# Kernel optimization log

Measured on AMD Instinct MI355X. Metric: run time of the kernel, lower is better.

Reference implementation:

```python
import jax, jax.numpy as jnp
import numpy as np

D_MODEL = 512
DFF = 2048
TOP_K = 2
EXPERTS_PER_LEVEL = (4, 8)  # hierarchical MoE: 2 levels


def setup_inputs() -> dict:
    key = jax.random.key(0)
    ks = jax.random.split(key, 12)
    def w(k, fan_in, shape):
        return jax.random.normal(k, shape, jnp.float32) * (1.0 / np.sqrt(fan_in))
    def b(k, shape):
        return jax.random.normal(k, shape, jnp.float32) * 0.01
    E0, E1 = EXPERTS_PER_LEVEL
    return {
        "x": jax.random.normal(ks[0], (4, 2048, D_MODEL), jnp.float32),
        # level 0: router + 4 experts (stacked along leading expert axis)
        "Wr0": w(ks[1], D_MODEL, (D_MODEL, E0)),
        "W1_0": w(ks[2], D_MODEL, (E0, D_MODEL, DFF)),
        "b1_0": b(ks[3], (E0, DFF)),
        "W2_0": w(ks[4], DFF, (E0, DFF, D_MODEL)),
        "b2_0": b(ks[5], (E0, D_MODEL)),
        # level 1: router + 8 experts
        "Wr1": w(ks[6], D_MODEL, (D_MODEL, E1)),
        "W1_1": w(ks[7], D_MODEL, (E1, D_MODEL, DFF)),
        "b1_1": b(ks[8], (E1, DFF)),
        "W2_1": w(ks[9], DFF, (E1, DFF, D_MODEL)),
        "b2_1": b(ks[10], (E1, D_MODEL)),
    }


def _moe_level(x, Wr, W1, b1, W2, b2, k):
    # Router: full softmax probs over experts; dispatch = binary top-k mask.
    probs = jax.nn.softmax(jnp.einsum('bsd,de->bse', x, Wr), axis=-1)  # [B,S,E]
    _, top_idx = jax.lax.top_k(probs, k)                               # [B,S,k]
    dispatch = jax.nn.one_hot(top_idx, probs.shape[-1], dtype=x.dtype).sum(axis=-2)  # [B,S,E]
    # Faithful to the source: every expert FFN runs on the MASKED inputs
    # (x * dispatch), then is combined with the FULL router probs.
    xm = x[:, :, None, :] * dispatch[..., None]                        # [B,S,E,D]
    h = jax.nn.relu(jnp.einsum('bsed,edf->bsef', xm, W1) + b1)         # [B,S,E,DFF]
    y = jnp.einsum('bsef,efd->bsed', h, W2) + b2                       # [B,S,E,D]
    return jnp.sum(y * probs[..., None], axis=2)                       # [B,S,D]


def reference(x, Wr0, W1_0, b1_0, W2_0, b2_0, Wr1, W1_1, b1_1, W2_1, b2_1):
    # inference path: dropout is identity, no capacity adaptation
    h0 = _moe_level(x, Wr0, W1_0, b1_0, W2_0, b2_0, TOP_K)
    out = _moe_level(h0, Wr1, W1_1, b1_1, W2_1, b2_1, TOP_K)
    return out
```

## Files before the change

kernel.cpp:

```cpp
#include <hip/hip_runtime.h>
#include <hip/hip_bf16.h>
#include <math.h>

#define TOK   8192
#define DM    512
#define DFFN  2048
#define NE0   4
#define NE1   8

typedef __bf16 bf16;
typedef __bf16 bf16x8 __attribute__((ext_vector_type(8)));
typedef float  f32x4  __attribute__((ext_vector_type(4)));

__device__ __forceinline__ double wave_sum_f64(double v){
#pragma unroll
  for (int o = 32; o > 0; o >>= 1) v += __shfl_down(v, o, 64);
  return v;
}
__device__ __forceinline__ float wave_sum_f32(float v){
#pragma unroll
  for (int o = 32; o > 0; o >>= 1) v += __shfl_down(v, o, 64);
  return v;
}

__device__ __forceinline__ void gload16(const bf16* g, bf16* l){
  __builtin_amdgcn_global_load_lds(
      (const __attribute__((address_space(1))) void*)g,
      (__attribute__((address_space(3))) void*)l, 16, 0, 0);
}

__global__ void f32_to_bf16(const float* __restrict__ in, bf16* __restrict__ out, int n){
  int i = blockIdx.x*256 + threadIdx.x;
  if (i < n) out[i] = (bf16)in[i];
}

__global__ void transpose_convert(const float* __restrict__ in, bf16* __restrict__ hi,
                                  bf16* __restrict__ lo, int K, int N){
  __shared__ float tile[64][65];
  int e  = blockIdx.z;
  int n0 = blockIdx.x*64, k0 = blockIdx.y*64;
  const float* src = in + (size_t)e*K*N;
  int c = threadIdx.x & 63, r4 = threadIdx.x >> 6;
#pragma unroll
  for (int i = 0; i < 16; ++i){
    int r = r4*16 + i;
    tile[r][c] = src[(size_t)(k0 + r)*N + n0 + c];
  }
  __syncthreads();
  bf16* dh = hi + (size_t)e*K*N;
  bf16* dl = lo ? (lo + (size_t)e*K*N) : nullptr;
#pragma unroll
  for (int i = 0; i < 16; ++i){
    int r = r4*16 + i;
    float v = tile[c][r];
    size_t o = (size_t)(n0 + r)*K + k0 + c;
    bf16 h = (bf16)v;
    dh[o] = h;
    if (dl) dl[o] = (bf16)(v - (float)h);
  }
}

__global__ void compute_c(const float* __restrict__ W2, const float* __restrict__ b1,
                          const float* __restrict__ b2, float* __restrict__ c){
  int gid = blockIdx.x*256 + threadIdx.x;
  int e = gid >> 9, d = gid & (DM-1);
  int fc = blockIdx.y;
  float acc = (fc == 0) ? b2[gid] : 0.f;
  const float* w  = W2 + (size_t)e*DFFN*DM + (size_t)fc*256*DM + d;
  const float* bb = b1 + e*DFFN + fc*256;
#pragma unroll 4
  for (int f = 0; f < 256; ++f) acc += fmaxf(bb[f], 0.f) * w[(size_t)f*DM];
  atomicAdd(&c[gid], acc);
}

__global__ void compute_M(const float* __restrict__ W2_0, const float* __restrict__ Wr1,
                          float* __restrict__ M, int nrows){
  int wv = threadIdx.x >> 6, lane = threadIdx.x & 63;
  int row = blockIdx.x*4 + wv;
  if (row >= nrows) return;
  const float* w = W2_0 + (size_t)row*DM + lane*8;
  float w8[8];
#pragma unroll
  for (int q = 0; q < 8; ++q) w8[q] = w[q];
  double acc[8] = {0,0,0,0,0,0,0,0};
#pragma unroll
  for (int q = 0; q < 8; ++q){
    const float* wr = Wr1 + (size_t)(lane*8 + q)*NE1;
#pragma unroll
    for (int p = 0; p < 8; ++p) acc[p] += (double)w8[q]*(double)wr[p];
  }
#pragma unroll
  for (int p = 0; p < 8; ++p) acc[p] = wave_sum_f64(acc[p]);
  if (lane == 0){
#pragma unroll
    for (int p = 0; p < 8; ++p) M[(size_t)row*8 + p] = (float)acc[p];
  }
}

__global__ void compute_cb_proj(const float* __restrict__ c0, const float* __restrict__ b2_0,
                                const float* __restrict__ Wr1, double* __restrict__ c0p,
                                double* __restrict__ b2p){
  int t = threadIdx.x;
  if (t >= NE0*NE1) return;
  int e = t >> 3, p = t & 7;
  double a = 0.0, b = 0.0;
  for (int d = 0; d < DM; ++d){
    double w = (double)Wr1[d*NE1 + p];
    a += (double)c0[e*DM + d]  * w;
    b += (double)b2_0[e*DM + d]* w;
  }
  c0p[t] = a; b2p[t] = b;
}

__global__ void prefix_offs(const int* __restrict__ counts, int NE, int* __restrict__ offs){
  if (threadIdx.x == 0){
    int s = 0;
    for (int e = 0; e < NE; ++e){ offs[e] = s; s += counts[e]; }
    offs[NE] = s;
  }
}

__global__ void router0_kernel(const float* __restrict__ x, const float* __restrict__ Wr0,
                               float* __restrict__ probs0, int* __restrict__ idx0,
                               bf16* __restrict__ xhi, bf16* __restrict__ xlo){
  int wv = threadIdx.x >> 6, lane = threadIdx.x & 63;
  int t = blockIdx.x*4 + wv;
  const float* xr = x + (size_t)t*DM + lane*8;
  float xv[8];
#pragma unroll
  for (int i = 0; i < 8; ++i) xv[i] = xr[i];
  bf16x8 hv, lv;
#pragma unroll
  for (int i = 0; i < 8; ++i){
    bf16 h = (bf16)xv[i];
    hv[i] = h;
    lv[i] = (bf16)(xv[i] - (float)h);
  }
  *(bf16x8*)(xhi + (size_t)t*DM + lane*8) = hv;
  *(bf16x8*)(xlo + (size_t)t*DM + lane*8) = lv;

  double lg[NE0];
#pragma unroll
  for (int e = 0; e < NE0; ++e){
    double s = 0.0;
#pragma unroll
    for (int i = 0; i < 8; ++i) s += (double)xv[i] * (double)Wr0[(lane*8 + i)*NE0 + e];
    lg[e] = wave_sum_f64(s);
  }
  if (lane == 0){
    double m = lg[0];
#pragma unroll
    for (int e = 1; e < NE0; ++e) m = fmax(m, lg[e]);
    double den = 0.0, ex[NE0];
#pragma unroll
    for (int e = 0; e < NE0; ++e){ ex[e] = exp(lg[e] - m); den += ex[e]; }
    float pf[NE0];
#pragma unroll
    for (int e = 0; e < NE0; ++e){ pf[e] = (float)(ex[e]/den); probs0[t*NE0 + e] = pf[e]; }
    int e0 = 0;
#pragma unroll
    for (int e = 1; e < NE0; ++e) if (pf[e] > pf[e0]) e0 = e;
    int e1 = (e0 == 0) ? 1 : 0;
#pragma unroll
    for (int e = 0; e < NE0; ++e) if (e != e0 && pf[e] > pf[e1]) e1 = e;
    idx0[t*2 + 0] = e0; idx0[t*2 + 1] = e1;
  }
}

__global__ void router1_kernel(const float* __restrict__ proj, const float* __restrict__ probs0,
                               const int* __restrict__ idx0, const double* __restrict__ c0p,
                               const double* __restrict__ b2p, float* __restrict__ probs1,
                               int* __restrict__ idx1){
  int t = blockIdx.x*256 + threadIdx.x;
  float p0[NE0];
#pragma unroll
  for (int e = 0; e < NE0; ++e) p0[e] = probs0[t*NE0 + e];
  double lg[NE1];
#pragma unroll
  for (int p = 0; p < NE1; ++p){
    double s = 0.0;
#pragma unroll
    for (int e = 0; e < NE0; ++e) s += (double)p0[e] * c0p[e*NE1 + p];
    lg[p] = s;
  }
#pragma unroll
  for (int sl = 0; sl < 2; ++sl){
    int e = idx0[t*2 + sl];
    double pe = (double)p0[e];
    const float* pr = proj + ((size_t)(sl*TOK + t))*NE1;
#pragma unroll
    for (int p = 0; p < NE1; ++p) lg[p] += pe * ((double)pr[p] + b2p[e*NE1 + p] - c0p[e*NE1 + p]);
  }
  double m = lg[0];
#pragma unroll
  for (int p = 1; p < NE1; ++p) m = fmax(m, lg[p]);
  double den = 0.0, ex[NE1];
#pragma unroll
  for (int p = 0; p < NE1; ++p){ ex[p] = exp(lg[p] - m); den += ex[p]; }
  float pf[NE1];
#pragma unroll
  for (int p = 0; p < NE1; ++p){ pf[p] = (float)(ex[p]/den); probs1[t*NE1 + p] = pf[p]; }
  int e0 = 0;
#pragma unroll
  for (int p = 1; p < NE1; ++p) if (pf[p] > pf[e0]) e0 = p;
  int e1 = (e0 == 0) ? 1 : 0;
#pragma unroll
  for (int p = 0; p < NE1; ++p) if (p != e0 && pf[p] > pf[e1]) e1 = p;
  idx1[t*2 + 0] = e0; idx1[t*2 + 1] = e1;
}

__global__ void build_lists(const int* __restrict__ idx, int NE,
                            int* __restrict__ list, int* __restrict__ counts){
  __shared__ int lcnt[8];
  __shared__ int lbase[8];
  const int tid = threadIdx.x, lane = tid & 63;
  if (tid < NE) lcnt[tid] = 0;
  __syncthreads();
  const int g = blockIdx.x*1024 + tid;
  const int slot = g >> 13;
  const int t = g & (TOK-1);
  const int e = idx[t*2 + slot];
  int wbase = 0, rank = 0;
  for (int ee = 0; ee < NE; ++ee){
    unsigned long long m = __ballot(e == ee);
    if (e == ee){
      int leader = __builtin_ctzll(m);
      int b = 0;
      if (lane == leader) b = atomicAdd(&lcnt[ee], (int)__popcll(m));
      wbase = __shfl(b, leader, 64);
      rank  = (int)__popcll(m & ((1ull << lane) - 1ull));
    }
  }
  __syncthreads();
  if (tid < NE) lbase[tid] = atomicAdd(&counts[tid], lcnt[tid]);
  __syncthreads();
  list[e*TOK + lbase[e] + wbase + rank] = slot*TOK + t;
}

__global__ void init_combine(const float* __restrict__ probs, const float* __restrict__ c,
                             int NE, float* __restrict__ tgt){
  int gid = blockIdx.x*256 + threadIdx.x;
  int t = gid >> 9, d = gid & (DM-1);
  float v = 0.f;
  for (int e = 0; e < NE; ++e) v += probs[t*NE + e] * c[e*DM + d];
  tgt[gid] = v;
}

__global__ void proj_from_h(const bf16* __restrict__ Hb, const bf16* __restrict__ Hlo,
                            int FC, int f0, const float* __restrict__ Mproj,
                            const int* __restrict__ list, const int* __restrict__ offs,
                            float* __restrict__ proj){
  int wv = threadIdx.x >> 6, lane = threadIdx.x & 63;
  int rr = blockIdx.x*4 + wv;
  if (rr >= offs[NE0]) return;
  int e = 0;
#pragma unroll
  for (int k = 1; k < NE0; ++k) if (rr >= offs[k]) e = k;
  int r = list[e*TOK + (rr - offs[e])];
  const bf16* hh = Hb  + (size_t)rr*FC;
  const bf16* hl = Hlo + (size_t)rr*FC;
  const float* Me = Mproj + ((size_t)e*DFFN + f0)*8;
  float acc[8] = {0,0,0,0,0,0,0,0};
  for (int c = 0; c < FC; c += 512){
    int fl = c + lane*8;
    if (fl < FC){
      bf16x8 a = *(const bf16x8*)(hh + fl);
      bf16x8 b = *(const bf16x8*)(hl + fl);
#pragma unroll
      for (int q = 0; q < 8; ++q){
        float hv = (float)a[q] + (float)b[q];
        const f32x4* mp = (const f32x4*)(Me + (size_t)(fl + q)*8);
        f32x4 m0 = mp[0], m1 = mp[1];
#pragma unroll
        for (int p = 0; p < 4; ++p){
          acc[p]   += hv * m0[p];
          acc[4+p] += hv * m1[p];
        }
      }
    }
  }
#pragma unroll
  for (int p = 0; p < 8; ++p) acc[p] = wave_sum_f32(acc[p]);
  if (lane == 0){
#pragma unroll
    for (int p = 0; p < 8; ++p) proj[(size_t)r*8 + p] += acc[p];
  }
}


template<int SPLIT>
__global__ __launch_bounds__(256, 2) void gemm_ffn1(
    const bf16* __restrict__ Ahi, const bf16* __restrict__ Alo,
    const bf16* __restrict__ Bhi, const bf16* __restrict__ Blo,
    const float* __restrict__ b1,
    const int* __restrict__ list, const int* __restrict__ counts,
    const int* __restrict__ offs,
    bf16* __restrict__ Hb, bf16* __restrict__ Hlo, int f0, int FC)
{
  constexpr int BUFE  = SPLIT ? 16384 : 8192;
  constexpr int SMEME = (2*BUFE > 17408) ? 2*BUFE : 17408;
  __shared__ alignas(16) bf16 smem[SMEME];

  const int e   = blockIdx.z;
  const int cnt = counts[e];
  const int bx = blockIdx.x, by = blockIdx.y;
  int xl, yl;
  if (gridDim.y == 16){
    xl = ((by >> 1) << 3) + (bx >> 3);
    yl = ((bx & 7) << 1) + (by & 1);
  } else { xl = bx; yl = by; }
  const int m0 = xl * 128;
  if (m0 >= cnt) return;
  const int rbase = offs[e] + m0;
  const int n0  = yl * 128;
  const int ng0 = f0 + n0;

  const int tid  = threadIdx.x;
  const int lane = tid & 63, wv = tid >> 6;
  const int wm = wv >> 1, wn = wv & 1;
  const int quad = lane >> 4, l15 = lane & 15;
  const int* le = list + e*TOK;

  const int strow = tid >> 2;
  const int ch8   = (((tid & 3) ^ ((tid >> 3) & 3)) << 3);
  int growR[2];
#pragma unroll
  for (int p = 0; p < 2; ++p){
    int m = m0 + p*64 + strow;
    growR[p] = (m < cnt) ? (le[m] & (TOK-1)) : 0;
  }
  const bf16* Bh = Bhi + (size_t)e*DFFN*DM;
  const bf16* Bl = SPLIT ? (Blo + (size_t)e*DFFN*DM) : nullptr;

  f32x4 acc[4][4];
#pragma unroll
  for (int i = 0; i < 4; ++i)
#pragma unroll
    for (int j = 0; j < 4; ++j) acc[i][j] = (f32x4){0.f,0.f,0.f,0.f};

  const int swzl = (l15 >> 1) & 3;
  int aPos[4], bPos[4];
#pragma unroll
  for (int i = 0; i < 4; ++i){
    aPos[i] = (wm*256 + (i*16 + l15)*4 + (quad ^ swzl)) * 8;
    bPos[i] = (wn*256 + (i*16 + l15)*4 + (quad ^ swzl)) * 8;
  }

  auto stage = [&](int ks, int buf){
    const int colo = (ks << 5) + ch8;
    bf16* dst = smem + buf*BUFE;
#pragma unroll
    for (int p = 0; p < 2; ++p){
      gload16(Ahi + (size_t)growR[p]*DM + colo,                  dst +         (p*256 + tid)*8);
      gload16(Bh  + (size_t)(ng0 + p*64 + strow)*DM + colo,      dst + 4096  + (p*256 + tid)*8);
      if (SPLIT){
        gload16(Alo + (size_t)growR[p]*DM + colo,                dst + 8192  + (p*256 + tid)*8);
        gload16(Bl  + (size_t)(ng0 + p*64 + strow)*DM + colo,    dst + 12288 + (p*256 + tid)*8);
      }
    }
  };

  constexpr int NIT = DM/32;
  stage(0, 0);
  stage(1, 1);
  int cur = 0;
  for (int ks = 0; ks < NIT; ++ks){
    if (ks + 1 < NIT){
      if (SPLIT) asm volatile("s_waitcnt vmcnt(8)" ::: "memory");
      else       asm volatile("s_waitcnt vmcnt(4)" ::: "memory");
    } else {
      asm volatile("s_waitcnt vmcnt(0)" ::: "memory");
    }
    __builtin_amdgcn_sched_barrier(0);
    __builtin_amdgcn_s_barrier();
    __builtin_amdgcn_sched_barrier(0);
    const bf16* B0 = smem + cur*BUFE;
    bf16x8 ah[4], bh[4];
#pragma unroll
    for (int i = 0; i < 4; ++i){
      ah[i] = *(const bf16x8*)&B0[aPos[i]];
      bh[i] = *(const bf16x8*)&B0[4096 + bPos[i]];
    }
#pragma unroll
    for (int i = 0; i < 4; ++i)
#pragma unroll
      for (int j = 0; j < 4; ++j)
        acc[i][j] = __builtin_amdgcn_mfma_f32_16x16x32_bf16(ah[i], bh[j], acc[i][j], 0,0,0);
    if (SPLIT){
      bf16x8 t2[4];
#pragma unroll
      for (int i = 0; i < 4; ++i) t2[i] = *(const bf16x8*)&B0[12288 + bPos[i]];
#pragma unroll
      for (int i = 0; i < 4; ++i)
#pragma unroll
        for (int j = 0; j < 4; ++j)
          acc[i][j] = __builtin_amdgcn_mfma_f32_16x16x32_bf16(ah[i], t2[j], acc[i][j], 0,0,0);
#pragma unroll
      for (int i = 0; i < 4; ++i) t2[i] = *(const bf16x8*)&B0[8192 + aPos[i]];
#pragma unroll
      for (int i = 0; i < 4; ++i)
#pragma unroll
        for (int j = 0; j < 4; ++j)
          acc[i][j] = __builtin_amdgcn_mfma_f32_16x16x32_bf16(t2[i], bh[j], acc[i][j], 0,0,0);
    }
    asm volatile("s_waitcnt lgkmcnt(0)" ::: "memory");
    __builtin_amdgcn_sched_barrier(0);
    __builtin_amdgcn_s_barrier();
    __builtin_amdgcn_sched_barrier(0);
    if (ks + 2 < NIT) stage(ks + 2, cur);
    cur ^= 1;
  }

  float bjv[4];
#pragma unroll
  for (int j = 0; j < 4; ++j)
    bjv[j] = b1[e*DFFN + ng0 + wn*64 + j*16 + l15];

  bf16* Cs = smem;
#pragma unroll
  for (int i = 0; i < 4; ++i)
#pragma unroll
    for (int j = 0; j < 4; ++j)
#pragma unroll
      for (int reg = 0; reg < 4; ++reg){
        float h = fmaxf(acc[i][j][reg] + bjv[j], 0.f);
        Cs[(wm*64 + i*16 + quad*4 + reg)*136 + wn*64 + j*16 + l15] = (bf16)h;
      }
  __syncthreads();
  {
    const int srow = tid >> 1, shalf = (tid & 1) * 64;
    if (m0 + srow < cnt){
      bf16* dst = Hb + (size_t)(rbase + srow)*FC + n0 + shalf;
      const bf16* srcl = &Cs[srow*136 + shalf];
#pragma unroll
      for (int q = 0; q < 8; ++q)
        *(bf16x8*)(dst + q*8) = *(const bf16x8*)(srcl + q*8);
    }
  }
  if (SPLIT){
    __syncthreads();
#pragma unroll
    for (int i = 0; i < 4; ++i)
#pragma unroll
      for (int j = 0; j < 4; ++j)
#pragma unroll
        for (int reg = 0; reg < 4; ++reg){
          float h = fmaxf(acc[i][j][reg] + bjv[j], 0.f);
          bf16 hi = (bf16)h;
          Cs[(wm*64 + i*16 + quad*4 + reg)*136 + wn*64 + j*16 + l15] = (bf16)(h - (float)hi);
        }
    __syncthreads();
    const int srow = tid >> 1, shalf = (tid & 1) * 64;
    if (m0 + srow < cnt){
      bf16* dst = Hlo + (size_t)(rbase + srow)*FC + n0 + shalf;
      const bf16* srcl = &Cs[srow*136 + shalf];
#pragma unroll
      for (int q = 0; q < 8; ++q)
        *(bf16x8*)(dst + q*8) = *(const bf16x8*)(srcl + q*8);
    }
  }
}

__global__ __launch_bounds__(256, 3) void gemm_ffn2(
    const bf16* __restrict__ Hb, int FC, int f0,
    const bf16* __restrict__ Bt,
    const float* __restrict__ b2, const float* __restrict__ ce,
    const float* __restrict__ probs, int NE,
    const int* __restrict__ list, const int* __restrict__ counts,
    const int* __restrict__ offs,
    float* __restrict__ tgt, int addBias)
{
  __shared__ alignas(16) bf16 smem[16384];

  const int e   = blockIdx.z;
  const int cnt = counts[e];
  const int bx = blockIdx.x, by = blockIdx.y;
  const int xl = (bx >> 3) + (((bx & 1) + (by << 1)) << 3);
  const int yl = (bx & 7) >> 1;
  const int m0 = xl*128;
  if (m0 >= cnt) return;
  const int rbase = offs[e];
  const int n0  = yl*128;

  const int tid = threadIdx.x, lane = tid & 63, wv = tid >> 6;
  const int wm = wv >> 1, wn = wv & 1, quad = lane >> 4, l15 = lane & 15;
  const int* le = list + e*TOK;

  const int strow = tid >> 2;
  const int ch8   = (((tid & 3) ^ ((tid >> 3) & 3)) << 3);
  int growR[2];
#pragma unroll
  for (int p = 0; p < 2; ++p){
    int m = m0 + p*64 + strow;
    growR[p] = rbase + ((m < cnt) ? m : (cnt - 1));
  }
  const bf16* Be = Bt + (size_t)e*DM*DFFN;

  f32x4 acc[4][4];
#pragma unroll
  for (int i = 0; i < 4; ++i)
#pragma unroll
    for (int j = 0; j < 4; ++j) acc[i][j] = (f32x4){0.f,0.f,0.f,0.f};

  const int swzl = (l15 >> 1) & 3;
  int aPos[4], bPos[4];
#pragma unroll
  for (int i = 0; i < 4; ++i){
    aPos[i] = (wm*256 + (i*16 + l15)*4 + (quad ^ swzl)) * 8;
    bPos[i] = (wn*256 + (i*16 + l15)*4 + (quad ^ swzl)) * 8;
  }

  auto stage = [&](int ks, int buf){
    const int colo = (ks << 5) + ch8;
    bf16* dst = smem + buf*8192;
#pragma unroll
    for (int p = 0; p < 2; ++p){
      gload16(Hb + (size_t)growR[p]*FC + colo,                       dst +        (p*256 + tid)*8);
      gload16(Be + (size_t)(n0 + p*64 + strow)*DFFN + f0 + colo,     dst + 4096 + (p*256 + tid)*8);
    }
  };

  const int NIT = FC/32;
  stage(0, 0);
  stage(1, 1);
  int cur = 0;
  for (int ks = 0; ks < NIT; ++ks){
    if (ks + 1 < NIT) asm volatile("s_waitcnt vmcnt(4)" ::: "memory");
    else              asm volatile("s_waitcnt vmcnt(0)" ::: "memory");
    __builtin_amdgcn_sched_barrier(0);
    __builtin_amdgcn_s_barrier();
    __builtin_amdgcn_sched_barrier(0);
    const bf16* B0 = smem + cur*8192;
    bf16x8 a[4], b[4];
#pragma unroll
    for (int i = 0; i < 4; ++i){
      a[i] = *(const bf16x8*)&B0[aPos[i]];
      b[i] = *(const bf16x8*)&B0[4096 + bPos[i]];
    }
#pragma unroll
    for (int i = 0; i < 4; ++i)
#pragma unroll
      for (int j = 0; j < 4; ++j)
        acc[i][j] = __builtin_amdgcn_mfma_f32_16x16x32_bf16(a[i], b[j], acc[i][j], 0,0,0);
    asm volatile("s_waitcnt lgkmcnt(0)" ::: "memory");
    __builtin_amdgcn_sched_barrier(0);
    __builtin_amdgcn_s_barrier();
    __builtin_amdgcn_sched_barrier(0);
    if (ks + 2 < NIT) stage(ks + 2, cur);
    cur ^= 1;
  }
#pragma unroll
  for (int i = 0; i < 4; ++i){
#pragma unroll
    for (int reg = 0; reg < 4; ++reg){
      int m = m0 + wm*64 + i*16 + quad*4 + reg;
      if (m >= cnt) continue;
      int r = le[m];
      int t = r & (TOK-1);
      float g = probs[t*NE + e];
#pragma unroll
      for (int j = 0; j < 4; ++j){
        int n = n0 + wn*64 + j*16 + l15;
        float v = acc[i][j][reg];
        if (addBias) v += b2[e*DM + n] - ce[e*DM + n];
        atomicAdd(&tgt[(size_t)t*DM + n], g*v);
      }
    }
  }
}

extern "C" void kernel_launch(void* const* d_in, const int* in_sizes, int n_in,
                              void* d_out, int out_size, void* d_ws, size_t ws_size,
                              hipStream_t stream)
{
  (void)in_sizes; (void)n_in; (void)out_size;
  const float* x    = (const float*)d_in[0];
  const float* Wr0  = (const float*)d_in[1];
  const float* W1_0 = (const float*)d_in[2];
  const float* b1_0 = (const float*)d_in[3];
  const float* W2_0 = (const float*)d_in[4];
  const float* b2_0 = (const float*)d_in[5];
  const float* Wr1  = (const float*)d_in[6];
  const float* W1_1 = (const float*)d_in[7];
  const float* b1_1 = (const float*)d_in[8];
  const float* W2_1 = (const float*)d_in[9];
  const float* b2_1 = (const float*)d_in[10];
  float* out = (float*)d_out;

  const size_t MB = (size_t)1 << 20;
  char* base = (char*)d_ws;

  bf16* xhi  = (bf16*)base;
  bf16* h0b  = (bf16*)base;
  bf16* xlo  = (bf16*)(base + 8*MB);
  bf16* w10h = (bf16*)(base + 16*MB);
  bf16* w10l = (bf16*)(base + 32*MB);
  bf16* w11h = (bf16*)(base + 16*MB);
  bf16* w21h = (bf16*)(base + 32*MB);
  bf16* w20h = (bf16*)(base + 48*MB);
  float* h0f = (float*)(base + 64*MB);

  char* mp = base + 80*MB;
  auto take = [&](size_t n) -> char* { char* p = mp; mp += (n + 255) & ~(size_t)255; return p; };
  float* probs0 = (float*)take((size_t)TOK*NE0*4);
  float* probs1 = (float*)take((size_t)TOK*NE1*4);
  int*   idx0   = (int*)  take((size_t)TOK*2*4);
  int*   idx1   = (int*)  take((size_t)TOK*2*4);
  int*   list0  = (int*)  take((size_t)NE0*TOK*4);
  int*   list1  = (int*)  take((size_t)NE1*TOK*4);
  int*   counts = (int*)  take(256);
  int*   offs0  = (int*)  take(256);
  int*   offs1  = (int*)  take(256);
  float* c0     = (float*)take((size_t)NE0*DM*4);
  float* c1     = (float*)take((size_t)NE1*DM*4);
  float* Mproj  = (float*)take((size_t)NE0*DFFN*NE1*4);
  double* c0p   = (double*)take(NE0*NE1*8);
  double* b2p   = (double*)take(NE0*NE1*8);
  float* proj   = (float*)take((size_t)2*TOK*NE1*4);

  const size_t fixed = 84*MB;
  int NCH;
  if      (ws_size >= fixed + 128*MB) NCH = 1;
  else if (ws_size >= fixed +  64*MB) NCH = 2;
  else if (ws_size >= fixed +  32*MB) NCH = 4;
  else if (ws_size >= fixed +  16*MB) NCH = 8;
  else return;
  const int FC = DFFN / NCH;
  const size_t chunkB = (size_t)2*TOK*FC*2;
  bf16* Hb   = (bf16*)(base + fixed);
  bf16* Hlo  = (bf16*)(base + fixed + chunkB);

  hipMemsetAsync(counts, 0, 16*sizeof(int), stream);
  hipMemsetAsync(c0, 0, (size_t)(NE0+NE1)*DM*4, stream);
  hipMemsetAsync(proj, 0, (size_t)2*TOK*NE1*4, stream);

  transpose_convert<<<dim3(DFFN/64, DM/64, NE0), 256, 0, stream>>>(W1_0, w10h, w10l, DM, DFFN);
  transpose_convert<<<dim3(DM/64, DFFN/64, NE0), 256, 0, stream>>>(W2_0, w20h, nullptr, DFFN, DM);
  compute_c<<<dim3(NE0*DM/256, 8), 256, 0, stream>>>(W2_0, b1_0, b2_0, c0);
  compute_c<<<dim3(NE1*DM/256, 8), 256, 0, stream>>>(W2_1, b1_1, b2_1, c1);
  compute_M<<<dim3(NE0*DFFN/4), 256, 0, stream>>>(W2_0, Wr1, Mproj, NE0*DFFN);
  compute_cb_proj<<<1, 64, 0, stream>>>(c0, b2_0, Wr1, c0p, b2p);

  router0_kernel<<<dim3(TOK/4), 256, 0, stream>>>(x, Wr0, probs0, idx0, xhi, xlo);
  build_lists<<<dim3(2*TOK/1024), 1024, 0, stream>>>(idx0, NE0, list0, counts);
  prefix_offs<<<1, 64, 0, stream>>>(counts, NE0, offs0);
  init_combine<<<dim3(TOK*DM/256), 256, 0, stream>>>(probs0, c0, NE0, h0f);
  for (int c = 0; c < NCH; ++c){
    gemm_ffn1<1><<<dim3(64, FC/128, NE0), 256, 0, stream>>>(
        xhi, xlo, w10h, w10l, b1_0, list0, counts, offs0, Hb, Hlo, c*FC, FC);
    proj_from_h<<<dim3(2*TOK/4), 256, 0, stream>>>(Hb, Hlo, FC, c*FC, Mproj,
                                                   list0, offs0, proj);
    gemm_ffn2<<<dim3(64, DM/128, NE0), 256, 0, stream>>>(
        Hb, FC, c*FC, w20h, b2_0, c0, probs0, NE0, list0, counts, offs0, h0f, (c == 0));
  }

  transpose_convert<<<dim3(DFFN/64, DM/64, NE1), 256, 0, stream>>>(W1_1, w11h, nullptr, DM, DFFN);
  transpose_convert<<<dim3(DM/64, DFFN/64, NE1), 256, 0, stream>>>(W2_1, w21h, nullptr, DFFN, DM);
  f32_to_bf16<<<dim3(TOK*DM/256), 256, 0, stream>>>(h0f, h0b, TOK*DM);
  router1_kernel<<<dim3(TOK/256), 256, 0, stream>>>(proj, probs0, idx0, c0p, b2p,
                                                    probs1, idx1);
  build_lists<<<dim3(2*TOK/1024), 1024, 0, stream>>>(idx1, NE1, list1, counts + NE0);
  prefix_offs<<<1, 64, 0, stream>>>(counts + NE0, NE1, offs1);
  init_combine<<<dim3(TOK*DM/256), 256, 0, stream>>>(probs1, c1, NE1, out);

  for (int c = 0; c < NCH; ++c){
    gemm_ffn1<0><<<dim3(64, FC/128, NE1), 256, 0, stream>>>(
        h0b, nullptr, w11h, nullptr, b1_1, list1, counts + NE0, offs1,
        Hb, nullptr, c*FC, FC);
    gemm_ffn2<<<dim3(64, DM/128, NE1), 256, 0, stream>>>(
        Hb, FC, c*FC, w21h, b2_1, c1, probs1, NE1, list1, counts + NE0, offs1, out, (c == 0));
  }
}
```

Measured before the change: 862.6 us.

## Replace atomic scatter-add in FFN2 epilogue with dense Y store plus gather combine

```diff
diff --git a/kernel.cpp b/kernel.cpp
--- a/kernel.cpp
+++ b/kernel.cpp
@@ -9,6 +9,7 @@
 #define NE1   8
 
 typedef __bf16 bf16;
+typedef __bf16 bf16x4 __attribute__((ext_vector_type(4)));
 typedef __bf16 bf16x8 __attribute__((ext_vector_type(8)));
 typedef float  f32x4  __attribute__((ext_vector_type(4)));
 
@@ -210,7 +211,8 @@
 }
 
 __global__ void build_lists(const int* __restrict__ idx, int NE,
-                            int* __restrict__ list, int* __restrict__ counts){
+                            int* __restrict__ list, int* __restrict__ counts,
+                            int* __restrict__ posn){
   __shared__ int lcnt[8];
   __shared__ int lbase[8];
   const int tid = threadIdx.x, lane = tid & 63;
@@ -234,7 +236,9 @@
   __syncthreads();
   if (tid < NE) lbase[tid] = atomicAdd(&counts[tid], lcnt[tid]);
   __syncthreads();
-  list[e*TOK + lbase[e] + wbase + rank] = slot*TOK + t;
+  const int p = lbase[e] + wbase + rank;
+  list[e*TOK + p] = slot*TOK + t;
+  posn[slot*TOK + t] = e*16384 + p;
 }
 
 __global__ void init_combine(const float* __restrict__ probs, const float* __restrict__ c,
@@ -244,6 +248,35 @@
   float v = 0.f;
   for (int e = 0; e < NE; ++e) v += probs[t*NE + e] * c[e*DM + d];
   tgt[gid] = v;
+}
+
+__global__ void gather_combine(const float* __restrict__ init, const float* __restrict__ Y,
+                               const int* __restrict__ posn, const int* __restrict__ offs,
+                               const float* __restrict__ probs, const float* __restrict__ b2,
+                               const float* __restrict__ ce, int NE,
+                               float* __restrict__ outF, bf16* __restrict__ outB){
+  int gid = blockIdx.x*256 + threadIdx.x;
+  int t = gid >> 7, d4 = (gid & 127) << 2;
+  f32x4 v = *(const f32x4*)(init + (size_t)t*DM + d4);
+#pragma unroll
+  for (int sl = 0; sl < 2; ++sl){
+    int pv = posn[sl*TOK + t];
+    int e = pv >> 14, p = pv & 16383;
+    int r = offs[e] + p;
+    float g = probs[t*NE + e];
+    f32x4 y  = *(const f32x4*)(Y  + (size_t)r*DM + d4);
+    f32x4 bb = *(const f32x4*)(b2 + (size_t)e*DM + d4);
+    f32x4 cc = *(const f32x4*)(ce + (size_t)e*DM + d4);
+#pragma unroll
+    for (int q = 0; q < 4; ++q) v[q] += g*(y[q] + bb[q] - cc[q]);
+  }
+  if (outF) *(f32x4*)(outF + (size_t)t*DM + d4) = v;
+  if (outB){
+    bf16x4 hb;
+#pragma unroll
+    for (int q = 0; q < 4; ++q) hb[q] = (bf16)v[q];
+    *(bf16x4*)(outB + (size_t)t*DM + d4) = hb;
+  }
 }
 
 __global__ void proj_from_h(const bf16* __restrict__ Hb, const bf16* __restrict__ Hlo,
@@ -468,7 +501,7 @@
     const float* __restrict__ probs, int NE,
     const int* __restrict__ list, const int* __restrict__ counts,
     const int* __restrict__ offs,
-    float* __restrict__ tgt, int addBias)
+    float* __restrict__ tgt, int addBias, float* __restrict__ Y)
 {
   __shared__ alignas(16) bf16 smem[16384];
 
@@ -549,21 +582,36 @@
     if (ks + 2 < NIT) stage(ks + 2, cur);
     cur ^= 1;
   }
-#pragma unroll
-  for (int i = 0; i < 4; ++i){
-#pragma unroll
-    for (int reg = 0; reg < 4; ++reg){
-      int m = m0 + wm*64 + i*16 + quad*4 + reg;
-      if (m >= cnt) continue;
-      int r = le[m];
-      int t = r & (TOK-1);
-      float g = probs[t*NE + e];
-#pragma unroll
-      for (int j = 0; j < 4; ++j){
-        int n = n0 + wn*64 + j*16 + l15;
-        float v = acc[i][j][reg];
-        if (addBias) v += b2[e*DM + n] - ce[e*DM + n];
-        atomicAdd(&tgt[(size_t)t*DM + n], g*v);
+  if (Y){
+#pragma unroll
+    for (int i = 0; i < 4; ++i){
+#pragma unroll
+      for (int reg = 0; reg < 4; ++reg){
+        int m = m0 + wm*64 + i*16 + quad*4 + reg;
+        if (m >= cnt) continue;
+        float* yr = Y + (size_t)(rbase + m)*DM + n0;
+#pragma unroll
+        for (int j = 0; j < 4; ++j)
+          yr[wn*64 + j*16 + l15] = acc[i][j][reg];
+      }
+    }
+  } else {
+#pragma unroll
+    for (int i = 0; i < 4; ++i){
+#pragma unroll
+      for (int reg = 0; reg < 4; ++reg){
+        int m = m0 + wm*64 + i*16 + quad*4 + reg;
+        if (m >= cnt) continue;
+        int r = le[m];
+        int t = r & (TOK-1);
+        float g = probs[t*NE + e];
+#pragma unroll
+        for (int j = 0; j < 4; ++j){
+          int n = n0 + wn*64 + j*16 + l15;
+          float v = acc[i][j][reg];
+          if (addBias) v += b2[e*DM + n] - ce[e*DM + n];
+          atomicAdd(&tgt[(size_t)t*DM + n], g*v);
+        }
       }
     }
   }
@@ -606,6 +654,8 @@
   float* probs1 = (float*)take((size_t)TOK*NE1*4);
   int*   idx0   = (int*)  take((size_t)TOK*2*4);
   int*   idx1   = (int*)  take((size_t)TOK*2*4);
+  int*   posn0  = (int*)  take((size_t)TOK*2*4);
+  int*   posn1  = (int*)  take((size_t)TOK*2*4);
   int*   list0  = (int*)  take((size_t)NE0*TOK*4);
   int*   list1  = (int*)  take((size_t)NE1*TOK*4);
   int*   counts = (int*)  take(256);
@@ -629,6 +679,8 @@
   const size_t chunkB = (size_t)2*TOK*FC*2;
   bf16* Hb   = (bf16*)(base + fixed);
   bf16* Hlo  = (bf16*)(base + fixed + chunkB);
+  const bool useY = (NCH == 1);
+  float* Ybuf = (float*)Hlo;
 
   hipMemsetAsync(counts, 0, 16*sizeof(int), stream);
   hipMemsetAsync(c0, 0, (size_t)(NE0+NE1)*DM*4, stream);
@@ -642,7 +694,7 @@
   compute_cb_proj<<<1, 64, 0, stream>>>(c0, b2_0, Wr1, c0p, b2p);
 
   router0_kernel<<<dim3(TOK/4), 256, 0, stream>>>(x, Wr0, probs0, idx0, xhi, xlo);
-  build_lists<<<dim3(2*TOK/1024), 1024, 0, stream>>>(idx0, NE0, list0, counts);
+  build_lists<<<dim3(2*TOK/1024), 1024, 0, stream>>>(idx0, NE0, list0, counts, posn0);
   prefix_offs<<<1, 64, 0, stream>>>(counts, NE0, offs0);
   init_combine<<<dim3(TOK*DM/256), 256, 0, stream>>>(probs0, c0, NE0, h0f);
   for (int c = 0; c < NCH; ++c){
@@ -651,15 +703,21 @@
     proj_from_h<<<dim3(2*TOK/4), 256, 0, stream>>>(Hb, Hlo, FC, c*FC, Mproj,
                                                    list0, offs0, proj);
     gemm_ffn2<<<dim3(64, DM/128, NE0), 256, 0, stream>>>(
-        Hb, FC, c*FC, w20h, b2_0, c0, probs0, NE0, list0, counts, offs0, h0f, (c == 0));
+        Hb, FC, c*FC, w20h, b2_0, c0, probs0, NE0, list0, counts, offs0, h0f, (c == 0),
+        useY ? Ybuf : nullptr);
   }
 
   transpose_convert<<<dim3(DFFN/64, DM/64, NE1), 256, 0, stream>>>(W1_1, w11h, nullptr, DM, DFFN);
   transpose_convert<<<dim3(DM/64, DFFN/64, NE1), 256, 0, stream>>>(W2_1, w21h, nullptr, DFFN, DM);
-  f32_to_bf16<<<dim3(TOK*DM/256), 256, 0, stream>>>(h0f, h0b, TOK*DM);
+  if (useY){
+    gather_combine<<<dim3(TOK*DM/4/256), 256, 0, stream>>>(
+        h0f, Ybuf, posn0, offs0, probs0, b2_0, c0, NE0, nullptr, h0b);
+  } else {
+    f32_to_bf16<<<dim3(TOK*DM/256), 256, 0, stream>>>(h0f, h0b, TOK*DM);
+  }
   router1_kernel<<<dim3(TOK/256), 256, 0, stream>>>(proj, probs0, idx0, c0p, b2p,
                                                     probs1, idx1);
-  build_lists<<<dim3(2*TOK/1024), 1024, 0, stream>>>(idx1, NE1, list1, counts + NE0);
+  build_lists<<<dim3(2*TOK/1024), 1024, 0, stream>>>(idx1, NE1, list1, counts + NE0, posn1);
   prefix_offs<<<1, 64, 0, stream>>>(counts + NE0, NE1, offs1);
   init_combine<<<dim3(TOK*DM/256), 256, 0, stream>>>(probs1, c1, NE1, out);
 
@@ -668,6 +726,11 @@
         h0b, nullptr, w11h, nullptr, b1_1, list1, counts + NE0, offs1,
         Hb, nullptr, c*FC, FC);
     gemm_ffn2<<<dim3(64, DM/128, NE1), 256, 0, stream>>>(
-        Hb, FC, c*FC, w21h, b2_1, c1, probs1, NE1, list1, counts + NE0, offs1, out, (c == 0));
-  }
-}
+        Hb, FC, c*FC, w21h, b2_1, c1, probs1, NE1, list1, counts + NE0, offs1, out, (c == 0),
+        useY ? Ybuf : nullptr);
+  }
+  if (useY){
+    gather_combine<<<dim3(TOK*DM/4/256), 256, 0, stream>>>(
+        out, Ybuf, posn1, offs1, probs1, b2_1, c1, NE1, out, nullptr);
+  }
+}
```

Measured after the change: 807.9 us. 1.07x faster.
